# Kernel optimization log

Hardware: AMD Instinct MI355X
Metric: run time of the kernel (lower is better)

## Reference

```python
import jax, jax.numpy as jnp
import numpy as np

NPOINT = 1024
RADIUS = 0.1
NSAMPLE = 32
EPS = 1e-5


def farthest_point_sample(xyz, npoint):
    # xyz: [B, N, 3] -> indices [B, npoint]
    B, N, _ = xyz.shape

    def step(carry, _):
        mind, far = carry  # [B,N], [B]
        centroid = jnp.take_along_axis(xyz, far[:, None, None], axis=1)  # [B,1,3]
        d = jnp.sum((xyz - centroid) ** 2, axis=-1)  # [B,N]
        mind = jnp.minimum(mind, d)
        return (mind, jnp.argmax(mind, axis=-1).astype(jnp.int32)), far

    init = (jnp.full((B, N), 1e10, xyz.dtype), jnp.zeros((B,), jnp.int32))
    _, idx = jax.lax.scan(step, init, None, length=npoint)  # [npoint, B]
    return idx.T


def ball_query(xyz, new_xyz, radius, nsample):
    # xyz [B,N,3], new_xyz [B,S,3] -> neighbor idx [B,S,nsample]
    N = xyz.shape[1]
    d2 = jnp.sum((new_xyz[:, :, None, :] - xyz[:, None, :, :]) ** 2, axis=-1)  # [B,S,N]
    idx = jnp.where(d2 <= radius ** 2, jnp.arange(N, dtype=jnp.int32), N)
    idx = jnp.sort(idx, axis=-1)[..., :nsample]
    first = idx[..., :1]  # center itself is always in-radius, so first is valid
    return jnp.where(idx == N, first, idx)


def _gather(x, idx):
    # x [B,N,C], idx [B,...] -> [B,...,C]
    return jax.vmap(lambda a, i: a[i])(x, idx)


def setup_inputs() -> dict:
    key = jax.random.key(0)
    ks = jax.random.split(key, 8)
    B, N, D = 16, 8192, 64
    inp = {
        "xyz": jax.random.uniform(ks[0], (B, 3, N), jnp.float32),
        "points": jax.random.normal(ks[1], (B, D, N), jnp.float32),
        "w0": jax.random.normal(ks[2], (64, 67), jnp.float32) * 0.05,
        "b0": jnp.zeros((64,), jnp.float32),
        "g0": jnp.ones((64,), jnp.float32),
        "beta0": jnp.zeros((64,), jnp.float32),
        "w1": jax.random.normal(ks[3], (64, 64), jnp.float32) * 0.05,
        "b1": jnp.zeros((64,), jnp.float32),
        "g1": jnp.ones((64,), jnp.float32),
        "beta1": jnp.zeros((64,), jnp.float32),
        "w2": jax.random.normal(ks[4], (128, 64), jnp.float32) * 0.05,
        "b2": jnp.zeros((128,), jnp.float32),
        "g2": jnp.ones((128,), jnp.float32),
        "beta2": jnp.zeros((128,), jnp.float32),
    }
    return inp


def reference(xyz, points, w0, b0, g0, beta0, w1, b1, g1, beta1, w2, b2, g2, beta2):
    # xyz [B,3,N], points [B,D,N]
    xyz_t = jnp.transpose(xyz, (0, 2, 1))      # [B,N,3]
    pts_t = jnp.transpose(points, (0, 2, 1))   # [B,N,D]

    fps_idx = farthest_point_sample(xyz_t, NPOINT)          # [B,S]
    new_xyz = _gather(xyz_t, fps_idx)                        # [B,S,3]
    gidx = ball_query(xyz_t, new_xyz, RADIUS, NSAMPLE)       # [B,S,K]

    grouped_xyz = _gather(xyz_t, gidx) - new_xyz[:, :, None, :]  # [B,S,K,3]
    grouped_pts = _gather(pts_t, gidx)                           # [B,S,K,D]
    feat = jnp.concatenate([grouped_xyz, grouped_pts], axis=-1)  # [B,S,K,3+D]
    B, S, K, C = feat.shape
    new_points = jnp.transpose(feat.reshape(B, S * K, C), (0, 2, 1))  # [B,C,S*K]

    for w, b, g, be in ((w0, b0, g0, beta0), (w1, b1, g1, beta1), (w2, b2, g2, beta2)):
        x = jnp.einsum('bcl,oc->bol', new_points, w) + b[None, :, None]
        mean = x.mean(axis=(0, 2), keepdims=True)
        var = x.var(axis=(0, 2), keepdims=True)
        new_points = jax.nn.relu(g[None, :, None] * (x - mean)
                                 * jax.lax.rsqrt(var + EPS) + be[None, :, None])

    new_points = jnp.max(new_points, axis=2)  # [B, mlp[-1]]
    return jnp.transpose(new_xyz, (0, 2, 1)), new_points
```

## Files before the change

kernel.cpp:

```cpp
#include <hip/hip_runtime.h>
#include <stdint.h>
#include <limits.h>

__device__ inline float mul_rn(float a, float b){ float r; asm("v_mul_f32 %0, %1, %2" : "=v"(r) : "v"(a), "v"(b)); return r; }
__device__ inline float add_rn(float a, float b){ float r; asm("v_add_f32 %0, %1, %2" : "=v"(r) : "v"(a), "v"(b)); return r; }
__device__ inline float sub_rn(float a, float b){ float r; asm("v_sub_f32 %0, %1, %2" : "=v"(r) : "v"(a), "v"(b)); return r; }

typedef uint16_t u16x8 __attribute__((ext_vector_type(8)));
typedef float    f32x2 __attribute__((ext_vector_type(2)));
typedef short    bf16x8 __attribute__((ext_vector_type(8)));
typedef float    fx4 __attribute__((ext_vector_type(4)));

__device__ inline float bf2f(uint16_t u){ return __uint_as_float(((uint32_t)u) << 16); }
__device__ inline uint16_t f2bf(float f){
    uint32_t u = __float_as_uint(f);
    u += 0x7fffu + ((u >> 16) & 1u);
    return (uint16_t)(u >> 16);
}
__device__ inline unsigned fkey(float f){
    unsigned u = __float_as_uint(f);
    return (u & 0x80000000u) ? ~u : (u | 0x80000000u);
}
__device__ inline float funkey(unsigned k){
    unsigned u = (k & 0x80000000u) ? (k ^ 0x80000000u) : ~k;
    return __uint_as_float(u);
}

__device__ inline unsigned dpp_umax_wave(unsigned v){
    unsigned t;
    t = (unsigned)__builtin_amdgcn_update_dpp((int)v, (int)v, 0x111, 0xf, 0xf, false); v = v > t ? v : t;
    t = (unsigned)__builtin_amdgcn_update_dpp((int)v, (int)v, 0x112, 0xf, 0xf, false); v = v > t ? v : t;
    t = (unsigned)__builtin_amdgcn_update_dpp((int)v, (int)v, 0x114, 0xf, 0xf, false); v = v > t ? v : t;
    t = (unsigned)__builtin_amdgcn_update_dpp((int)v, (int)v, 0x118, 0xf, 0xf, false); v = v > t ? v : t;
    t = (unsigned)__builtin_amdgcn_update_dpp((int)v, (int)v, 0x142, 0xf, 0xf, false); v = v > t ? v : t;
    t = (unsigned)__builtin_amdgcn_update_dpp((int)v, (int)v, 0x143, 0xf, 0xf, false); v = v > t ? v : t;
    return v;
}

#define NPTS   8192
#define NBATCH 16
#define NPOINT 1024
#define NSAMP  32
#define LCOLS  32768
#define NTOT   524288.0f
#define NBUCK  32

#define OFF_FPS   0u
#define OFF_GIDX  65536u
#define OFF_SSC   2162688u
#define OFF_MM    2263040u
#define OFF_WPK0  2279424u
#define OFF_WPK1  2291712u
#define OFF_WPK2  2299904u
#define OFF_T0    4194304u
#define OFF_PTST  138412032u

__global__ __launch_bounds__(512) void fps_fused_kernel(const float* __restrict__ xyz,
        int* __restrict__ fps_idx, float* __restrict__ out_xyz,
        const float* __restrict__ pts, uint16_t* __restrict__ ptsT,
        const float* __restrict__ w0, const float* __restrict__ w1, const float* __restrict__ w2,
        uint16_t* __restrict__ wpk0, uint16_t* __restrict__ wpk1, uint16_t* __restrict__ wpk2){
#pragma clang fp contract(off)
    __shared__ __align__(16) float smem[33824];
    const int bid = blockIdx.x, tid = threadIdx.x;

    if (bid >= 2064){
        int t = (bid - 2064) * 512 + tid;
        if (t < 64*96){
            int o = t / 96, cp = t % 96;
            uint16_t v = 0;
            if (cp < 64)      v = f2bf(w0[o*67 + (cp + 3)]);
            else if (cp < 67) v = f2bf(w0[o*67 + (cp - 64)]);
            wpk0[((cp>>3)*64 + o)*8 + (cp&7)] = v;
        }
        if (t < 64*64){ int o = t >> 6, c = t & 63; wpk1[((c>>3)*64  + o)*8 + (c&7)] = f2bf(w1[t]); }
        if (t < 128*64){ int o = t >> 6, c = t & 63; wpk2[((c>>3)*128 + o)*8 + (c&7)] = f2bf(w2[t]); }
        return;
    }
    if (bid >= 16){
        float (*tile)[65] = (float(*)[65])smem;
        const int tb = bid - 16;
        const int bt = tb >> 7, n0 = (tb & 127) << 6;
        const int tn = tid & 63, tg = tid >> 6;
        const float* src = pts + (size_t)bt * 64 * NPTS + n0;
#pragma unroll
        for (int i = 0; i < 8; i++){ int c = tg*8 + i; tile[c][tn] = src[(size_t)c * NPTS + tn]; }
        __syncthreads();
        uint16_t* dst = ptsT + ((size_t)bt * NPTS + n0) * 64;
#pragma unroll
        for (int i = 0; i < 8; i++){ int n = tg*8 + i; dst[(size_t)n * 64 + tn] = f2bf(tile[tn][n]); }
        return;
    }

    float* sxyz = smem;
    float4* sxyz4 = (float4*)smem;
    unsigned long long* wslots = (unsigned long long*)(smem + 32768);
    int* sidx = (int*)(smem + 32800);
    const int b = bid;
    const float* px = xyz + (size_t)b * 3 * NPTS;
    for (int i = tid; i < NPTS; i += 512)
        sxyz4[i] = float4{px[i], px[NPTS + i], px[2*NPTS + i], 0.f};
    __syncthreads();

    const int p0 = tid << 4;
    const float4* rp = sxyz4 + p0;
    f32x2 X2[8], Y2[8], Z2[8], M2[8];
#pragma unroll
    for (int j = 0; j < 8; j++){
        float4 qa = rp[2*j], qb = rp[2*j + 1];
        X2[j] = f32x2{qa.x, qb.x};
        Y2[j] = f32x2{qa.y, qb.y};
        Z2[j] = f32x2{qa.z, qb.z};
        M2[j] = f32x2{1e10f, 1e10f};
    }
    const unsigned base = ~(unsigned)p0;

    int cur = 0;
    float cx = sxyz[0], cy = sxyz[1], cz = sxyz[2];
    for (int t = 0; t < NPOINT; t++){
        if (tid == 0) sidx[t] = cur;
        const f32x2 c2x = f32x2{cx, cx}, c2y = f32x2{cy, cy}, c2z = f32x2{cz, cz};
#pragma unroll
        for (int j = 0; j < 8; j++){
            f32x2 dx = X2[j] - c2x;
            f32x2 dy = Y2[j] - c2y;
            f32x2 dz = Z2[j] - c2z;
            f32x2 d2 = dx*dx + dy*dy + dz*dz;
            M2[j].x = fminf(M2[j].x, d2.x);
            M2[j].y = fminf(M2[j].y, d2.y);
        }
        float tv[8];
#pragma unroll
        for (int j = 0; j < 8; j++) tv[j] = fmaxf(M2[j].x, M2[j].y);
        float t0_ = fmaxf(fmaxf(tv[0], tv[1]), fmaxf(tv[2], tv[3]));
        float t1_ = fmaxf(fmaxf(tv[4], tv[5]), fmaxf(tv[6], tv[7]));
        const float mt = fmaxf(t0_, t1_);
        unsigned jpos = 0;
#pragma unroll
        for (int j = 7; j >= 0; j--){
            if (M2[j].y == mt) jpos = 2*j + 1;
            if (M2[j].x == mt) jpos = 2*j;
        }
        const unsigned lo = base - jpos;
        const unsigned mtu = __float_as_uint(mt);
        unsigned vm = dpp_umax_wave(mtu);
        const unsigned wvu = __builtin_amdgcn_readlane(vm, 63);
        unsigned long long cand = __ballot(mtu == wvu);
        const int fl = __ffsll((long long)cand) - 1;
        const unsigned wlo = __builtin_amdgcn_readlane(lo, fl);
        if ((tid & 63) == 0)
            wslots[(t & 1) * 8 + (tid >> 6)] = (((unsigned long long)wvu) << 32) | wlo;
        __syncthreads();
        const ulonglong2* sp = (const ulonglong2*)(wslots + (t & 1) * 8);
        ulonglong2 ka = sp[0], kb = sp[1], kc = sp[2], kd = sp[3];
        unsigned long long ma = (ka.y > ka.x) ? ka.y : ka.x;
        unsigned long long mb = (kb.y > kb.x) ? kb.y : kb.x;
        unsigned long long mc = (kc.y > kc.x) ? kc.y : kc.x;
        unsigned long long md = (kd.y > kd.x) ? kd.y : kd.x;
        unsigned long long mab = (mb > ma) ? mb : ma;
        unsigned long long mcd = (md > mc) ? md : mc;
        unsigned long long win = (mcd > mab) ? mcd : mab;
        cur = (int)(~((unsigned)win));
        const float4 cc4 = sxyz4[cur];
        cx = cc4.x; cy = cc4.y; cz = cc4.z;
    }
    __syncthreads();
#pragma unroll
    for (int q = 0; q < 2; q++){
        const int i = (q << 9) + tid;
        const int idx = sidx[i];
        fps_idx[b * NPOINT + i] = idx;
        const float4 c4 = sxyz4[idx];
        float* oxp = out_xyz + b * 3 * NPOINT;
        oxp[i]            = c4.x;
        oxp[NPOINT + i]   = c4.y;
        oxp[2*NPOINT + i] = c4.z;
    }
}

__global__ __launch_bounds__(256) void ballquery_kernel(const float* __restrict__ xyz,
                                                        const int* __restrict__ fps_idx, int* __restrict__ gidx){
    const int w = (blockIdx.x << 2) + (threadIdx.x >> 6);
    const int lane = threadIdx.x & 63;
    const int b = w >> 10, s = w & 1023;
    const float* px = xyz + (size_t)b * 3 * NPTS;
    const int ci = fps_idx[b * NPOINT + s];
    const float cx = px[ci], cy = px[NPTS+ci], cz = px[2*NPTS+ci];
    int* gout = gidx + (size_t)b * LCOLS + s * NSAMP;
    const unsigned long long lmask = (1ull << lane) - 1ull;
    int have = 0, first_p = 0; bool got = false;
    for (int c0 = 0; c0 < NPTS; c0 += 128){
        const int pA = c0 + lane, pB = c0 + 64 + lane;
        const float xA = px[pA], yA = px[NPTS+pA], zA = px[2*NPTS+pA];
        const float xB = px[pB], yB = px[NPTS+pB], zB = px[2*NPTS+pB];
        {
            float dx = sub_rn(xA, cx), dy = sub_rn(yA, cy), dz = sub_rn(zA, cz);
            float d2 = add_rn(add_rn(mul_rn(dx,dx), mul_rn(dy,dy)), mul_rn(dz,dz));
            bool in = (d2 <= 0.01f);
            unsigned long long m = __ballot(in);
            if (m && !got){ first_p = c0 + __ffsll((long long)m) - 1; got = true; }
            if (in){
                int pos = have + __popcll(m & lmask);
                if (pos < NSAMP) gout[pos] = pA;
            }
            have += __popcll(m);
        }
        {
            float dx = sub_rn(xB, cx), dy = sub_rn(yB, cy), dz = sub_rn(zB, cz);
            float d2 = add_rn(add_rn(mul_rn(dx,dx), mul_rn(dy,dy)), mul_rn(dz,dz));
            bool in = (d2 <= 0.01f);
            unsigned long long m = __ballot(in);
            if (m && !got){ first_p = c0 + 64 + __ffsll((long long)m) - 1; got = true; }
            if (in){
                int pos = have + __popcll(m & lmask);
                if (pos < NSAMP) gout[pos] = pB;
            }
            have += __popcll(m);
        }
    }
    for (int pos = have + lane; pos < NSAMP; pos += 64) gout[pos] = first_p;
}

__global__ __launch_bounds__(256) void mfma_mm0_kernel(
        const float* __restrict__ xyz, const float* __restrict__ nx,
        const uint16_t* __restrict__ ptsT, const int* __restrict__ gidx,
        const uint16_t* __restrict__ wpack, const float* __restrict__ bias,
        uint16_t* __restrict__ xout, float* __restrict__ ssc){
    __shared__ __align__(16) uint16_t sB[12 * 256 * 8];
    __shared__ __align__(16) uint16_t sA[12 * 64 * 8];
    __shared__ float sb_[64];
    __shared__ float sred_s[4][64], sred_ss[4][64];
    const int tid = threadIdx.x;
    const int b = blockIdx.x >> 7;
    const int n0 = (blockIdx.x & 127) << 8;

    if (tid < 64) sb_[tid] = bias[tid];
    for (int i = tid; i < 12*64; i += 256) *(u16x8*)&sA[i*8] = *(const u16x8*)&wpack[i*8];
    __syncthreads();
    {
        const int ls = n0 + tid;
        const int s = ls >> 5;
        const int g = gidx[(size_t)b * LCOLS + ls];
        const float* px = xyz + (size_t)b * 3 * NPTS;
        float f0 = sub_rn(px[g],        nx[b*3*NPOINT + s]);
        float f1 = sub_rn(px[NPTS+g],   nx[b*3*NPOINT + NPOINT + s]);
        float f2 = sub_rn(px[2*NPTS+g], nx[b*3*NPOINT + 2*NPOINT + s]);
        const u16x8* pr = (const u16x8*)(ptsT + ((size_t)b * NPTS + (size_t)g) * 64);
#pragma unroll
        for (int kc = 0; kc < 8; kc++) *(u16x8*)&sB[(kc*256 + tid)*8] = pr[kc];
        u16x8 xrow; xrow[0] = f2bf(f0); xrow[1] = f2bf(f1); xrow[2] = f2bf(f2);
        xrow[3] = 0; xrow[4] = 0; xrow[5] = 0; xrow[6] = 0; xrow[7] = 0;
        *(u16x8*)&sB[(8*256 + tid)*8] = xrow;
        u16x8 zr; zr[0]=0;zr[1]=0;zr[2]=0;zr[3]=0;zr[4]=0;zr[5]=0;zr[6]=0;zr[7]=0;
#pragma unroll
        for (int kc = 9; kc < 12; kc++) *(u16x8*)&sB[(kc*256 + tid)*8] = zr;
    }
    __syncthreads();

    const int lane = tid & 63, w = tid >> 6;
    const int lhi = lane >> 4, llo = lane & 15;
    fx4 acc[4][4];
#pragma unroll
    for (int mt = 0; mt < 4; mt++)
#pragma unroll
        for (int nt = 0; nt < 4; nt++) acc[mt][nt] = fx4{0.f,0.f,0.f,0.f};

#pragma unroll
    for (int kk = 0; kk < 3; kk++){
        bf16x8 bfrag[4];
#pragma unroll
        for (int nt = 0; nt < 4; nt++){
            int n = w * 64 + nt * 16 + llo;
            bfrag[nt] = *(const bf16x8*)&sB[((kk*4 + lhi) * 256 + n) * 8];
        }
#pragma unroll
        for (int mt = 0; mt < 4; mt++){
            bf16x8 afrag = *(const bf16x8*)&sA[((kk*4 + lhi) * 64 + mt*16 + llo) * 8];
#pragma unroll
            for (int nt = 0; nt < 4; nt++)
                acc[mt][nt] = __builtin_amdgcn_mfma_f32_16x16x32_bf16(afrag, bfrag[nt], acc[mt][nt], 0, 0, 0);
        }
    }
#pragma unroll
    for (int mt = 0; mt < 4; mt++){
#pragma unroll
        for (int j = 0; j < 4; j++){
            const int ch = mt*16 + lhi*4 + j;
            const float bv = sb_[ch];
            float a0 = acc[mt][0][j] + bv, a1 = acc[mt][1][j] + bv;
            float a2 = acc[mt][2][j] + bv, a3 = acc[mt][3][j] + bv;
            uint16_t* op = xout + (size_t)b * 64 * LCOLS + (size_t)ch * LCOLS + n0 + w*64 + llo;
            op[0]  = f2bf(a0); op[16] = f2bf(a1); op[32] = f2bf(a2); op[48] = f2bf(a3);
            float s  = (a0 + a1) + (a2 + a3);
            float ss = fmaf(a0, a0, fmaf(a1, a1, fmaf(a2, a2, a3*a3)));
#pragma unroll
            for (int off = 1; off < 16; off <<= 1){ s += __shfl_xor(s, off); ss += __shfl_xor(ss, off); }
            if (llo == 0){ sred_s[w][ch] = s; sred_ss[w][ch] = ss; }
        }
    }
    __syncthreads();
    if (tid < 64){
        float s  = sred_s[0][tid]  + sred_s[1][tid]  + sred_s[2][tid]  + sred_s[3][tid];
        float ss = sred_ss[0][tid] + sred_ss[1][tid] + sred_ss[2][tid] + sred_ss[3][tid];
        float* sbck = ssc + (blockIdx.x & (NBUCK-1)) * 256;
        atomicAdd(&sbck[tid], s);
        atomicAdd(&sbck[128 + tid], ss);
    }
}

__global__ __launch_bounds__(256) void mfma_stats1_kernel(
        const uint16_t* __restrict__ xin, const uint16_t* __restrict__ wpack,
        const float* __restrict__ bias,
        const float* __restrict__ pssc, const float* __restrict__ pg, const float* __restrict__ pbeta,
        float* __restrict__ ssc){
    __shared__ __align__(16) uint16_t sB[8 * 256 * 8];
    __shared__ __align__(16) uint16_t sA[8 * 64 * 8];
    __shared__ float sa_[64], sc_[64], sb_[64];
    __shared__ float sred_s[4][64], sred_ss[4][64];
    const int tid = threadIdx.x;
    const int b = blockIdx.x >> 7;
    const int n0 = (blockIdx.x & 127) << 8;

    if (tid < 64){
        float s = 0.f, ss = 0.f;
#pragma unroll 4
        for (int k = 0; k < NBUCK; k++){ s += pssc[k*256 + tid]; ss += pssc[k*256 + 128 + tid]; }
        const float inv = 1.0f / NTOT;
        float mean = s * inv;
        float var  = ss * inv - mean * mean;
        float a = pg[tid] / sqrtf(var + 1e-5f);
        sa_[tid] = a;
        sc_[tid] = fmaf(-mean, a, pbeta[tid]);
        sb_[tid] = bias[tid];
    }
    for (int i = tid; i < 64*8; i += 256) *(u16x8*)&sA[i*8] = *(const u16x8*)&wpack[i*8];
    __syncthreads();
    {
        const uint16_t* xp = xin + (size_t)b * 64 * LCOLS + (n0 + tid);
#pragma unroll 8
        for (int c = 0; c < 64; c++){
            float v = bf2f(xp[(size_t)c * LCOLS]);
            v = fmaxf(fmaf(sa_[c], v, sc_[c]), 0.0f);
            sB[((c >> 3) * 256 + tid) * 8 + (c & 7)] = f2bf(v);
        }
    }
    __syncthreads();
    const int lane = tid & 63, w = tid >> 6;
    const int lhi = lane >> 4, llo = lane & 15;
    fx4 acc[4][4];
#pragma unroll
    for (int mt = 0; mt < 4; mt++)
#pragma unroll
        for (int nt = 0; nt < 4; nt++) acc[mt][nt] = fx4{0.f,0.f,0.f,0.f};
#pragma unroll
    for (int kk = 0; kk < 2; kk++){
        bf16x8 bfrag[4];
#pragma unroll
        for (int nt = 0; nt < 4; nt++){
            int n = w * 64 + nt * 16 + llo;
            bfrag[nt] = *(const bf16x8*)&sB[((kk*4 + lhi) * 256 + n) * 8];
        }
#pragma unroll
        for (int mt = 0; mt < 4; mt++){
            bf16x8 afrag = *(const bf16x8*)&sA[((kk*4 + lhi) * 64 + mt*16 + llo) * 8];
#pragma unroll
            for (int nt = 0; nt < 4; nt++)
                acc[mt][nt] = __builtin_amdgcn_mfma_f32_16x16x32_bf16(afrag, bfrag[nt], acc[mt][nt], 0, 0, 0);
        }
    }
#pragma unroll
    for (int mt = 0; mt < 4; mt++){
#pragma unroll
        for (int j = 0; j < 4; j++){
            const int ch = mt*16 + lhi*4 + j;
            const float bv = sb_[ch];
            float a0 = acc[mt][0][j] + bv, a1 = acc[mt][1][j] + bv;
            float a2 = acc[mt][2][j] + bv, a3 = acc[mt][3][j] + bv;
            float s  = (a0 + a1) + (a2 + a3);
            float ss = fmaf(a0, a0, fmaf(a1, a1, fmaf(a2, a2, a3*a3)));
#pragma unroll
            for (int off = 1; off < 16; off <<= 1){ s += __shfl_xor(s, off); ss += __shfl_xor(ss, off); }
            if (llo == 0){ sred_s[w][ch] = s; sred_ss[w][ch] = ss; }
        }
    }
    __syncthreads();
    if (tid < 64){
        float s  = sred_s[0][tid]  + sred_s[1][tid]  + sred_s[2][tid]  + sred_s[3][tid];
        float ss = sred_ss[0][tid] + sred_ss[1][tid] + sred_ss[2][tid] + sred_ss[3][tid];
        float* sbck = ssc + (blockIdx.x & (NBUCK-1)) * 256;
        atomicAdd(&sbck[tid], s);
        atomicAdd(&sbck[128 + tid], ss);
    }
}

__global__ __launch_bounds__(256) void mfma_mm12_kernel(
        const uint16_t* __restrict__ xin,
        const uint16_t* __restrict__ wpk1, const uint16_t* __restrict__ wpk2,
        const float* __restrict__ b1, const float* __restrict__ b2,
        const float* __restrict__ ssc0, const float* __restrict__ g0, const float* __restrict__ be0,
        const float* __restrict__ ssc1, const float* __restrict__ g1, const float* __restrict__ be1,
        float* __restrict__ ssc2, unsigned* __restrict__ mmax, unsigned* __restrict__ mmin){
    __shared__ __align__(16) uint16_t sB[8 * 256 * 8];
    __shared__ __align__(16) uint16_t sA1[8 * 64 * 8];
    __shared__ __align__(16) uint16_t sA2[8 * 128 * 8];
    __shared__ float sa0_[64], sc0_[64], sa1_[64], sc1_[64], sb1_[64], sb2_[128];
    __shared__ float sred_s[4][128], sred_ss[4][128], sred_mx[4][128], sred_mn[4][128];
    const int tid = threadIdx.x;
    const int b = blockIdx.x >> 7;
    const int n0 = (blockIdx.x & 127) << 8;

    if (tid < 64){
        float s0 = 0.f, ss0 = 0.f, s1 = 0.f, ss1 = 0.f;
#pragma unroll 4
        for (int k = 0; k < NBUCK; k++){
            s0 += ssc0[k*256 + tid]; ss0 += ssc0[k*256 + 128 + tid];
            s1 += ssc1[k*256 + tid]; ss1 += ssc1[k*256 + 128 + tid];
        }
        const float inv = 1.0f / NTOT;
        float m0 = s0 * inv, v0 = ss0 * inv - m0*m0;
        float a0 = g0[tid] / sqrtf(v0 + 1e-5f);
        sa0_[tid] = a0; sc0_[tid] = fmaf(-m0, a0, be0[tid]);
        float m1 = s1 * inv, v1 = ss1 * inv - m1*m1;
        float a1 = g1[tid] / sqrtf(v1 + 1e-5f);
        sa1_[tid] = a1; sc1_[tid] = fmaf(-m1, a1, be1[tid]);
        sb1_[tid] = b1[tid];
    }
    if (tid < 128) sb2_[tid] = b2[tid];
    for (int i = tid; i < 64*8; i += 256)  *(u16x8*)&sA1[i*8] = *(const u16x8*)&wpk1[i*8];
    for (int i = tid; i < 128*8; i += 256) *(u16x8*)&sA2[i*8] = *(const u16x8*)&wpk2[i*8];
    __syncthreads();
    {
        const uint16_t* xp = xin + (size_t)b * 64 * LCOLS + (n0 + tid);
#pragma unroll 8
        for (int c = 0; c < 64; c++){
            float v = bf2f(xp[(size_t)c * LCOLS]);
            v = fmaxf(fmaf(sa0_[c], v, sc0_[c]), 0.0f);
            sB[((c >> 3) * 256 + tid) * 8 + (c & 7)] = f2bf(v);
        }
    }
    __syncthreads();
    const int lane = tid & 63, w = tid >> 6;
    const int lhi = lane >> 4, llo = lane & 15;

    fx4 acc1[4][4];
#pragma unroll
    for (int mt = 0; mt < 4; mt++)
#pragma unroll
        for (int nt = 0; nt < 4; nt++) acc1[mt][nt] = fx4{0.f,0.f,0.f,0.f};
#pragma unroll
    for (int kk = 0; kk < 2; kk++){
        bf16x8 bfrag[4];
#pragma unroll
        for (int nt = 0; nt < 4; nt++){
            int n = w * 64 + nt * 16 + llo;
            bfrag[nt] = *(const bf16x8*)&sB[((kk*4 + lhi) * 256 + n) * 8];
        }
#pragma unroll
        for (int mt = 0; mt < 4; mt++){
            bf16x8 afrag = *(const bf16x8*)&sA1[((kk*4 + lhi) * 64 + mt*16 + llo) * 8];
#pragma unroll
            for (int nt = 0; nt < 4; nt++)
                acc1[mt][nt] = __builtin_amdgcn_mfma_f32_16x16x32_bf16(afrag, bfrag[nt], acc1[mt][nt], 0, 0, 0);
        }
    }
    __syncthreads();

#pragma unroll
    for (int mt = 0; mt < 4; mt++){
#pragma unroll
        for (int j = 0; j < 4; j++){
            const int ch = mt*16 + lhi*4 + j;
            const float bv = sb1_[ch], av = sa1_[ch], cv = sc1_[ch];
#pragma unroll
            for (int nt = 0; nt < 4; nt++){
                float z = fmaxf(fmaf(av, acc1[mt][nt][j] + bv, cv), 0.0f);
                int n = w*64 + nt*16 + llo;
                sB[((ch >> 3) * 256 + n) * 8 + (ch & 7)] = f2bf(z);
            }
        }
    }
    __syncthreads();

    fx4 acc2[8][4];
#pragma unroll
    for (int mt = 0; mt < 8; mt++)
#pragma unroll
        for (int nt = 0; nt < 4; nt++) acc2[mt][nt] = fx4{0.f,0.f,0.f,0.f};
#pragma unroll
    for (int kk = 0; kk < 2; kk++){
        bf16x8 bfrag[4];
#pragma unroll
        for (int nt = 0; nt < 4; nt++){
            int n = w * 64 + nt * 16 + llo;
            bfrag[nt] = *(const bf16x8*)&sB[((kk*4 + lhi) * 256 + n) * 8];
        }
#pragma unroll
        for (int mt = 0; mt < 8; mt++){
            bf16x8 afrag = *(const bf16x8*)&sA2[((kk*4 + lhi) * 128 + mt*16 + llo) * 8];
#pragma unroll
            for (int nt = 0; nt < 4; nt++)
                acc2[mt][nt] = __builtin_amdgcn_mfma_f32_16x16x32_bf16(afrag, bfrag[nt], acc2[mt][nt], 0, 0, 0);
        }
    }
#pragma unroll
    for (int mt = 0; mt < 8; mt++){
#pragma unroll
        for (int j = 0; j < 4; j++){
            const int ch = mt*16 + lhi*4 + j;
            const float bv = sb2_[ch];
            float a0 = acc2[mt][0][j] + bv, a1 = acc2[mt][1][j] + bv;
            float a2 = acc2[mt][2][j] + bv, a3 = acc2[mt][3][j] + bv;
            float s  = (a0 + a1) + (a2 + a3);
            float ss = fmaf(a0, a0, fmaf(a1, a1, fmaf(a2, a2, a3*a3)));
            float mx = fmaxf(fmaxf(a0, a1), fmaxf(a2, a3));
            float mn = fminf(fminf(a0, a1), fminf(a2, a3));
#pragma unroll
            for (int off = 1; off < 16; off <<= 1){
                s += __shfl_xor(s, off); ss += __shfl_xor(ss, off);
                mx = fmaxf(mx, __shfl_xor(mx, off)); mn = fminf(mn, __shfl_xor(mn, off));
            }
            if (llo == 0){ sred_s[w][ch] = s; sred_ss[w][ch] = ss; sred_mx[w][ch] = mx; sred_mn[w][ch] = mn; }
        }
    }
    __syncthreads();
    if (tid < 128){
        float s  = sred_s[0][tid]  + sred_s[1][tid]  + sred_s[2][tid]  + sred_s[3][tid];
        float ss = sred_ss[0][tid] + sred_ss[1][tid] + sred_ss[2][tid] + sred_ss[3][tid];
        float mx = fmaxf(fmaxf(sred_mx[0][tid], sred_mx[1][tid]), fmaxf(sred_mx[2][tid], sred_mx[3][tid]));
        float mn = fminf(fminf(sred_mn[0][tid], sred_mn[1][tid]), fminf(sred_mn[2][tid], sred_mn[3][tid]));
        float* sbck = ssc2 + (blockIdx.x & (NBUCK-1)) * 256;
        atomicAdd(&sbck[tid], s);
        atomicAdd(&sbck[128 + tid], ss);
        atomicMax(&mmax[b * 128 + tid], fkey(mx));
        atomicMin(&mmin[b * 128 + tid], fkey(mn));
    }
}

__global__ __launch_bounds__(64) void final_kernel(const float* __restrict__ ssc, const float* __restrict__ g2,
                                                   const float* __restrict__ be2, const unsigned* __restrict__ mmax,
                                                   const unsigned* __restrict__ mmin, float* __restrict__ out){
    const int t = blockIdx.x * 64 + threadIdx.x;
    const int o = t & 127;
    float s = 0.f, ss = 0.f;
    for (int k = 0; k < NBUCK; k++){ s += ssc[k*256 + o]; ss += ssc[k*256 + 128 + o]; }
    const float inv = 1.0f / NTOT;
    float mean = s * inv;
    float var  = ss * inv - mean * mean;
    float a = g2[o] / sqrtf(var + 1e-5f);
    float c = fmaf(-mean, a, be2[o]);
    unsigned k = (a >= 0.f) ? mmax[t] : mmin[t];
    float x = funkey(k);
    out[49152 + t] = fmaxf(fmaf(a, x, c), 0.0f);
}

extern "C" void kernel_launch(void* const* d_in, const int* in_sizes, int n_in,
                              void* d_out, int out_size, void* d_ws, size_t ws_size,
                              hipStream_t stream){
    const float* xyz = (const float*)d_in[0];
    const float* pts = (const float*)d_in[1];
    const float* w0  = (const float*)d_in[2];  const float* b0  = (const float*)d_in[3];
    const float* g0  = (const float*)d_in[4];  const float* be0 = (const float*)d_in[5];
    const float* w1  = (const float*)d_in[6];  const float* b1  = (const float*)d_in[7];
    const float* g1  = (const float*)d_in[8];  const float* be1 = (const float*)d_in[9];
    const float* w2  = (const float*)d_in[10]; const float* b2  = (const float*)d_in[11];
    const float* g2  = (const float*)d_in[12]; const float* be2 = (const float*)d_in[13];
    float* out = (float*)d_out;
    char* ws = (char*)d_ws;

    int*      fps_idx = (int*)(ws + OFF_FPS);
    int*      gidx    = (int*)(ws + OFF_GIDX);
    float*    ssc0    = (float*)(ws + OFF_SSC);
    float*    ssc1    = ssc0 + NBUCK*256;
    float*    ssc2    = ssc1 + NBUCK*256;
    unsigned* mmax    = (unsigned*)(ws + OFF_MM);
    unsigned* mmin    = mmax + 2048;
    uint16_t* wpk0    = (uint16_t*)(ws + OFF_WPK0);
    uint16_t* wpk1    = (uint16_t*)(ws + OFF_WPK1);
    uint16_t* wpk2    = (uint16_t*)(ws + OFF_WPK2);
    uint16_t* t0      = (uint16_t*)(ws + OFF_T0);
    uint16_t* ptsT    = (uint16_t*)(ws + OFF_PTST);

    hipMemsetAsync(ws + OFF_SSC, 0, 3 * NBUCK * 256 * 4, stream);
    hipMemsetAsync(ws + OFF_MM, 0x00, 8192, stream);
    hipMemsetAsync(ws + OFF_MM + 8192, 0xFF, 8192, stream);

    fps_fused_kernel<<<2080, 512, 0, stream>>>(xyz, fps_idx, out, pts, ptsT,
                                               w0, w1, w2, wpk0, wpk1, wpk2);
    ballquery_kernel<<<4096, 256, 0, stream>>>(xyz, fps_idx, gidx);

    mfma_mm0_kernel<<<2048, 256, 0, stream>>>(xyz, out, ptsT, gidx, wpk0, b0, t0, ssc0);

    mfma_stats1_kernel<<<2048, 256, 0, stream>>>(t0, wpk1, b1, ssc0, g0, be0, ssc1);

    mfma_mm12_kernel<<<2048, 256, 0, stream>>>(t0, wpk1, wpk2, b1, b2,
                                               ssc0, g0, be0, ssc1, g1, be1,
                                               ssc2, mmax, mmin);

    final_kernel<<<32, 64, 0, stream>>>(ssc2, g2, be2, mmax, mmin, out);
}
```

Baseline: 1.149 ms.

## Process two batches per FPS block and fetch centroids from global memory

Each FPS block now runs farthest-point sampling for two batch items at once and shares one barrier per iteration between them. The intent is to halve the number of serial barriers per item and to interleave two independent dependency chains inside one block. The shared-memory copy of xyz is removed: points load straight from global into registers, and each iteration's centroid is read from global/L2, which adds latency to the critical path. Register pressure doubles, and only eight blocks now carry the serial FPS work.

```diff
diff --git a/kernel.cpp b/kernel.cpp
--- a/kernel.cpp
+++ b/kernel.cpp
@@ -61,11 +61,11 @@
         const float* __restrict__ w0, const float* __restrict__ w1, const float* __restrict__ w2,
         uint16_t* __restrict__ wpk0, uint16_t* __restrict__ wpk1, uint16_t* __restrict__ wpk2){
 #pragma clang fp contract(off)
-    __shared__ __align__(16) float smem[33824];
+    __shared__ __align__(16) float smem[4224];
     const int bid = blockIdx.x, tid = threadIdx.x;
 
-    if (bid >= 2064){
-        int t = (bid - 2064) * 512 + tid;
+    if (bid >= 2056){
+        int t = (bid - 2056) * 512 + tid;
         if (t < 64*96){
             int o = t / 96, cp = t % 96;
             uint16_t v = 0;
@@ -77,9 +77,9 @@
         if (t < 128*64){ int o = t >> 6, c = t & 63; wpk2[((c>>3)*128 + o)*8 + (c&7)] = f2bf(w2[t]); }
         return;
     }
-    if (bid >= 16){
+    if (bid >= 8){
         float (*tile)[65] = (float(*)[65])smem;
-        const int tb = bid - 16;
+        const int tb = bid - 8;
         const int bt = tb >> 7, n0 = (tb & 127) << 6;
         const int tn = tid & 63, tg = tid >> 6;
         const float* src = pts + (size_t)bt * 64 * NPTS + n0;
@@ -92,89 +92,153 @@
         return;
     }
 
-    float* sxyz = smem;
-    float4* sxyz4 = (float4*)smem;
-    unsigned long long* wslots = (unsigned long long*)(smem + 32768);
-    int* sidx = (int*)(smem + 32800);
-    const int b = bid;
-    const float* px = xyz + (size_t)b * 3 * NPTS;
-    for (int i = tid; i < NPTS; i += 512)
-        sxyz4[i] = float4{px[i], px[NPTS + i], px[2*NPTS + i], 0.f};
-    __syncthreads();
+    int* sidxA = (int*)smem;
+    int* sidxB = (int*)(smem + 1024);
+    unsigned long long* slots = (unsigned long long*)(smem + 2048);
+    const float* pxA = xyz + (size_t)(2*bid)     * 3 * NPTS;
+    const float* pxB = xyz + (size_t)(2*bid + 1) * 3 * NPTS;
 
     const int p0 = tid << 4;
-    const float4* rp = sxyz4 + p0;
-    f32x2 X2[8], Y2[8], Z2[8], M2[8];
-#pragma unroll
-    for (int j = 0; j < 8; j++){
-        float4 qa = rp[2*j], qb = rp[2*j + 1];
-        X2[j] = f32x2{qa.x, qb.x};
-        Y2[j] = f32x2{qa.y, qb.y};
-        Z2[j] = f32x2{qa.z, qb.z};
-        M2[j] = f32x2{1e10f, 1e10f};
-    }
+    f32x2 XA[8], YA[8], ZA[8], MA[8], XB[8], YB[8], ZB[8], MB[8];
+#pragma unroll
+    for (int k = 0; k < 4; k++){
+        float4 qx = *(const float4*)(pxA + p0 + 4*k);
+        float4 qy = *(const float4*)(pxA + NPTS + p0 + 4*k);
+        float4 qz = *(const float4*)(pxA + 2*NPTS + p0 + 4*k);
+        XA[2*k] = f32x2{qx.x, qx.y}; XA[2*k+1] = f32x2{qx.z, qx.w};
+        YA[2*k] = f32x2{qy.x, qy.y}; YA[2*k+1] = f32x2{qy.z, qy.w};
+        ZA[2*k] = f32x2{qz.x, qz.y}; ZA[2*k+1] = f32x2{qz.z, qz.w};
+        qx = *(const float4*)(pxB + p0 + 4*k);
+        qy = *(const float4*)(pxB + NPTS + p0 + 4*k);
+        qz = *(const float4*)(pxB + 2*NPTS + p0 + 4*k);
+        XB[2*k] = f32x2{qx.x, qx.y}; XB[2*k+1] = f32x2{qx.z, qx.w};
+        YB[2*k] = f32x2{qy.x, qy.y}; YB[2*k+1] = f32x2{qy.z, qy.w};
+        ZB[2*k] = f32x2{qz.x, qz.y}; ZB[2*k+1] = f32x2{qz.z, qz.w};
+    }
+#pragma unroll
+    for (int j = 0; j < 8; j++){ MA[j] = f32x2{1e10f, 1e10f}; MB[j] = f32x2{1e10f, 1e10f}; }
     const unsigned base = ~(unsigned)p0;
 
-    int cur = 0;
-    float cx = sxyz[0], cy = sxyz[1], cz = sxyz[2];
+    int curA = 0, curB = 0;
+    float cxA = pxA[0], cyA = pxA[NPTS], czA = pxA[2*NPTS];
+    float cxB = pxB[0], cyB = pxB[NPTS], czB = pxB[2*NPTS];
+
     for (int t = 0; t < NPOINT; t++){
-        if (tid == 0) sidx[t] = cur;
-        const f32x2 c2x = f32x2{cx, cx}, c2y = f32x2{cy, cy}, c2z = f32x2{cz, cz};
-#pragma unroll
-        for (int j = 0; j < 8; j++){
-            f32x2 dx = X2[j] - c2x;
-            f32x2 dy = Y2[j] - c2y;
-            f32x2 dz = Z2[j] - c2z;
-            f32x2 d2 = dx*dx + dy*dy + dz*dz;
-            M2[j].x = fminf(M2[j].x, d2.x);
-            M2[j].y = fminf(M2[j].y, d2.y);
-        }
-        float tv[8];
-#pragma unroll
-        for (int j = 0; j < 8; j++) tv[j] = fmaxf(M2[j].x, M2[j].y);
-        float t0_ = fmaxf(fmaxf(tv[0], tv[1]), fmaxf(tv[2], tv[3]));
-        float t1_ = fmaxf(fmaxf(tv[4], tv[5]), fmaxf(tv[6], tv[7]));
-        const float mt = fmaxf(t0_, t1_);
-        unsigned jpos = 0;
-#pragma unroll
-        for (int j = 7; j >= 0; j--){
-            if (M2[j].y == mt) jpos = 2*j + 1;
-            if (M2[j].x == mt) jpos = 2*j;
-        }
-        const unsigned lo = base - jpos;
-        const unsigned mtu = __float_as_uint(mt);
-        unsigned vm = dpp_umax_wave(mtu);
-        const unsigned wvu = __builtin_amdgcn_readlane(vm, 63);
-        unsigned long long cand = __ballot(mtu == wvu);
-        const int fl = __ffsll((long long)cand) - 1;
-        const unsigned wlo = __builtin_amdgcn_readlane(lo, fl);
-        if ((tid & 63) == 0)
-            wslots[(t & 1) * 8 + (tid >> 6)] = (((unsigned long long)wvu) << 32) | wlo;
+        if (tid == 0){ sidxA[t] = curA; sidxB[t] = curB; }
+        {
+            const f32x2 c2x = f32x2{cxA, cxA}, c2y = f32x2{cyA, cyA}, c2z = f32x2{czA, czA};
+#pragma unroll
+            for (int j = 0; j < 8; j++){
+                f32x2 dx = XA[j] - c2x;
+                f32x2 dy = YA[j] - c2y;
+                f32x2 dz = ZA[j] - c2z;
+                f32x2 d2 = dx*dx + dy*dy + dz*dz;
+                MA[j].x = fminf(MA[j].x, d2.x);
+                MA[j].y = fminf(MA[j].y, d2.y);
+            }
+            float tv[8];
+#pragma unroll
+            for (int j = 0; j < 8; j++) tv[j] = fmaxf(MA[j].x, MA[j].y);
+            float t0_ = fmaxf(fmaxf(tv[0], tv[1]), fmaxf(tv[2], tv[3]));
+            float t1_ = fmaxf(fmaxf(tv[4], tv[5]), fmaxf(tv[6], tv[7]));
+            const float mt = fmaxf(t0_, t1_);
+            unsigned jpos = 0;
+#pragma unroll
+            for (int j = 7; j >= 0; j--){
+                if (MA[j].y == mt) jpos = 2*j + 1;
+                if (MA[j].x == mt) jpos = 2*j;
+            }
+            const unsigned lo = base - jpos;
+            const unsigned mtu = __float_as_uint(mt);
+            unsigned vm = dpp_umax_wave(mtu);
+            const unsigned wvu = __builtin_amdgcn_readlane(vm, 63);
+            unsigned long long cand = __ballot(mtu == wvu);
+            const int fl = __ffsll((long long)cand) - 1;
+            const unsigned wlo = __builtin_amdgcn_readlane(lo, fl);
+            if ((tid & 63) == 0)
+                slots[(t & 1) * 16 + (tid >> 6)] = (((unsigned long long)wvu) << 32) | wlo;
+        }
+        {
+            const f32x2 c2x = f32x2{cxB, cxB}, c2y = f32x2{cyB, cyB}, c2z = f32x2{czB, czB};
+#pragma unroll
+            for (int j = 0; j < 8; j++){
+                f32x2 dx = XB[j] - c2x;
+                f32x2 dy = YB[j] - c2y;
+                f32x2 dz = ZB[j] - c2z;
+                f32x2 d2 = dx*dx + dy*dy + dz*dz;
+                MB[j].x = fminf(MB[j].x, d2.x);
+                MB[j].y = fminf(MB[j].y, d2.y);
+            }
+            float tv[8];
+#pragma unroll
+            for (int j = 0; j < 8; j++) tv[j] = fmaxf(MB[j].x, MB[j].y);
+            float t0_ = fmaxf(fmaxf(tv[0], tv[1]), fmaxf(tv[2], tv[3]));
+            float t1_ = fmaxf(fmaxf(tv[4], tv[5]), fmaxf(tv[6], tv[7]));
+            const float mt = fmaxf(t0_, t1_);
+            unsigned jpos = 0;
+#pragma unroll
+            for (int j = 7; j >= 0; j--){
+                if (MB[j].y == mt) jpos = 2*j + 1;
+                if (MB[j].x == mt) jpos = 2*j;
+            }
+            const unsigned lo = base - jpos;
+            const unsigned mtu = __float_as_uint(mt);
+            unsigned vm = dpp_umax_wave(mtu);
+            const unsigned wvu = __builtin_amdgcn_readlane(vm, 63);
+            unsigned long long cand = __ballot(mtu == wvu);
+            const int fl = __ffsll((long long)cand) - 1;
+            const unsigned wlo = __builtin_amdgcn_readlane(lo, fl);
+            if ((tid & 63) == 0)
+                slots[(t & 1) * 16 + 8 + (tid >> 6)] = (((unsigned long long)wvu) << 32) | wlo;
+        }
         __syncthreads();
-        const ulonglong2* sp = (const ulonglong2*)(wslots + (t & 1) * 8);
-        ulonglong2 ka = sp[0], kb = sp[1], kc = sp[2], kd = sp[3];
-        unsigned long long ma = (ka.y > ka.x) ? ka.y : ka.x;
-        unsigned long long mb = (kb.y > kb.x) ? kb.y : kb.x;
-        unsigned long long mc = (kc.y > kc.x) ? kc.y : kc.x;
-        unsigned long long md = (kd.y > kd.x) ? kd.y : kd.x;
-        unsigned long long mab = (mb > ma) ? mb : ma;
-        unsigned long long mcd = (md > mc) ? md : mc;
-        unsigned long long win = (mcd > mab) ? mcd : mab;
-        cur = (int)(~((unsigned)win));
-        const float4 cc4 = sxyz4[cur];
-        cx = cc4.x; cy = cc4.y; cz = cc4.z;
+        {
+            const ulonglong2* sp = (const ulonglong2*)(slots + (t & 1) * 16);
+            ulonglong2 ka = sp[0], kb = sp[1], kc = sp[2], kd = sp[3];
+            unsigned long long ma = (ka.y > ka.x) ? ka.y : ka.x;
+            unsigned long long mb = (kb.y > kb.x) ? kb.y : kb.x;
+            unsigned long long mc = (kc.y > kc.x) ? kc.y : kc.x;
+            unsigned long long md = (kd.y > kd.x) ? kd.y : kd.x;
+            unsigned long long mab = (mb > ma) ? mb : ma;
+            unsigned long long mcd = (md > mc) ? md : mc;
+            unsigned long long win = (mcd > mab) ? mcd : mab;
+            curA = (int)(~((unsigned)win));
+            cxA = pxA[curA]; cyA = pxA[NPTS + curA]; czA = pxA[2*NPTS + curA];
+        }
+        {
+            const ulonglong2* sp = (const ulonglong2*)(slots + (t & 1) * 16 + 8);
+            ulonglong2 ka = sp[0], kb = sp[1], kc = sp[2], kd = sp[3];
+            unsigned long long ma = (ka.y > ka.x) ? ka.y : ka.x;
+            unsigned long long mb = (kb.y > kb.x) ? kb.y : kb.x;
+            unsigned long long mc = (kc.y > kc.x) ? kc.y : kc.x;
+            unsigned long long md = (kd.y > kd.x) ? kd.y : kd.x;
+            unsigned long long mab = (mb > ma) ? mb : ma;
+            unsigned long long mcd = (md > mc) ? md : mc;
+            unsigned long long win = (mcd > mab) ? mcd : mab;
+            curB = (int)(~((unsigned)win));
+            cxB = pxB[curB]; cyB = pxB[NPTS + curB]; czB = pxB[2*NPTS + curB];
+        }
     }
     __syncthreads();
 #pragma unroll
     for (int q = 0; q < 2; q++){
         const int i = (q << 9) + tid;
-        const int idx = sidx[i];
-        fps_idx[b * NPOINT + i] = idx;
-        const float4 c4 = sxyz4[idx];
-        float* oxp = out_xyz + b * 3 * NPOINT;
-        oxp[i]            = c4.x;
-        oxp[NPOINT + i]   = c4.y;
-        oxp[2*NPOINT + i] = c4.z;
+        {
+            const int idx = sidxA[i];
+            fps_idx[(2*bid) * NPOINT + i] = idx;
+            float* oxp = out_xyz + (size_t)(2*bid) * 3 * NPOINT;
+            oxp[i]            = pxA[idx];
+            oxp[NPOINT + i]   = pxA[NPTS + idx];
+            oxp[2*NPOINT + i] = pxA[2*NPTS + idx];
+        }
+        {
+            const int idx = sidxB[i];
+            fps_idx[(2*bid + 1) * NPOINT + i] = idx;
+            float* oxp = out_xyz + (size_t)(2*bid + 1) * 3 * NPOINT;
+            oxp[i]            = pxB[idx];
+            oxp[NPOINT + i]   = pxB[NPTS + idx];
+            oxp[2*NPOINT + i] = pxB[2*NPTS + idx];
+        }
     }
 }
 
@@ -584,7 +648,7 @@
     hipMemsetAsync(ws + OFF_MM, 0x00, 8192, stream);
     hipMemsetAsync(ws + OFF_MM + 8192, 0xFF, 8192, stream);
 
-    fps_fused_kernel<<<2080, 512, 0, stream>>>(xyz, fps_idx, out, pts, ptsT,
+    fps_fused_kernel<<<2072, 512, 0, stream>>>(xyz, fps_idx, out, pts, ptsT,
                                                w0, w1, w2, wpk0, wpk1, wpk2);
     ballquery_kernel<<<4096, 256, 0, stream>>>(xyz, fps_idx, gidx);
 
```

After: 2.054 ms. 78.9% more time.
